# Kernel tuning notes

Hardware: AMD Instinct MI355X
Metric: run time of the kernel (lower is better)

Reference implementation:

```python
import jax, jax.numpy as jnp
import numpy as np

R_MAX = 2.0
DR_MIN = 0.02
N_ATOMS = 200000
N_EDGES = 12800000

def setup_inputs() -> dict:
    key = jax.random.key(0)
    k1, k2, k3, k4, k5, k6 = jax.random.split(key, 6)
    R = jax.random.normal(k1, (N_ATOMS, 3), dtype=jnp.float32)
    dr_vec = jax.random.normal(k2, (N_EDGES, 3), dtype=jnp.float32)
    Z = jax.random.randint(k3, (N_ATOMS,), 0, 119, dtype=jnp.int32)
    idx = jax.random.randint(k4, (2, N_EDGES), 0, N_ATOMS, dtype=jnp.int32)
    box = jnp.zeros((3, 3), dtype=jnp.float32)
    rep_scale = jax.random.uniform(k5, (119,), dtype=jnp.float32, minval=0.2, maxval=1.8)
    rep_prefactor = jax.random.uniform(k6, (119,), dtype=jnp.float32, minval=0.5, maxval=2.0)
    return {"R": R, "dr_vec": dr_vec, "Z": Z, "idx": idx, "box": box,
            "properties": 0, "rep_scale": rep_scale, "rep_prefactor": rep_prefactor}

def reference(R, dr_vec, Z, idx, box, properties, rep_scale, rep_prefactor):
    idx_i, idx_j = idx[0], idx[1]
    # gather per-edge atomic numbers, then per-element parameters
    Z_i = Z[idx_i]
    Z_j = Z[idx_j]
    # per-edge distance, clipped to [0.02, r_max]
    dr = jnp.sqrt(jnp.sum(dr_vec * dr_vec, axis=-1)).astype(jnp.float32)
    dr = jnp.clip(dr, 0.02, R_MAX)
    cos_cutoff = 0.5 * (jnp.cos(np.pi * dr / R_MAX) + 1.0)
    A_i = jnp.abs(rep_prefactor[Z_i])
    A_j = jnp.abs(rep_prefactor[Z_j])
    R_i = jnp.abs(rep_scale[Z_i])
    R_j = jnp.abs(rep_scale[Z_j])
    f = A_i * A_j * jnp.exp(-dr * (R_i + R_j) / (R_i * R_j)) / (dr * dr)
    E_ij = f * cos_cutoff
    # mask padding/self edges (apax pads neighbor lists with idx_i == idx_j)
    mask = (idx_i != idx_j).astype(E_ij.dtype)
    E_ij = E_ij * mask
    # fp64_sum in original; high-precision accumulation via plain sum here
    E = jnp.sum(E_ij)
    return E
```

## Files before the change

### kernel.cpp

```cpp
#include <hip/hip_runtime.h>
#include <hip/hip_bf16.h>
#include <hip/hip_fp16.h>

#define RMAXF 2.0f
#define PI_F 3.14159265358979f

typedef float f32x4 __attribute__((ext_vector_type(4)));
typedef int   i32x4 __attribute__((ext_vector_type(4)));

__global__ __launch_bounds__(256) void build_params(
    const int*   __restrict__ Z,
    const float* __restrict__ rep_scale,
    const float* __restrict__ rep_prefactor,
    __half2*     __restrict__ parh,
    int n_atoms)
{
    int a = blockIdx.x * blockDim.x + threadIdx.x;
    if (a < n_atoms) {
        int z = Z[a];
        float A = fabsf(rep_prefactor[z]);
        float S = 1.0f / fabsf(rep_scale[z]);
        parh[a] = __floats2half2_rn(A, S);
    }
}

__global__ __launch_bounds__(256) void edge_kernel(
    const f32x4* __restrict__ dr4,
    const i32x4* __restrict__ idx_i4,
    const i32x4* __restrict__ idx_j4,
    const __half2* __restrict__ parh,
    float*        __restrict__ out,
    int n_oct, int n_edges)
{
    int q = blockIdx.x * blockDim.x + threadIdx.x;
    float acc = 0.0f;

    if (q < n_oct) {
        f32x4 va = __builtin_nontemporal_load(&dr4[6 * q + 0]);
        f32x4 vb = __builtin_nontemporal_load(&dr4[6 * q + 1]);
        f32x4 vc = __builtin_nontemporal_load(&dr4[6 * q + 2]);
        f32x4 vd = __builtin_nontemporal_load(&dr4[6 * q + 3]);
        f32x4 ve = __builtin_nontemporal_load(&dr4[6 * q + 4]);
        f32x4 vg = __builtin_nontemporal_load(&dr4[6 * q + 5]);
        i32x4 ia = __builtin_nontemporal_load(&idx_i4[2 * q + 0]);
        i32x4 ib = __builtin_nontemporal_load(&idx_i4[2 * q + 1]);
        i32x4 ja = __builtin_nontemporal_load(&idx_j4[2 * q + 0]);
        i32x4 jb = __builtin_nontemporal_load(&idx_j4[2 * q + 1]);

        int ii[8] = { ia.x, ia.y, ia.z, ia.w, ib.x, ib.y, ib.z, ib.w };
        int jj[8] = { ja.x, ja.y, ja.z, ja.w, jb.x, jb.y, jb.z, jb.w };

        __half2 hi[8], hj[8];
        #pragma unroll
        for (int k = 0; k < 8; ++k) { hi[k] = parh[ii[k]]; hj[k] = parh[jj[k]]; }

        float d2[8];
        d2[0] = va.x * va.x + va.y * va.y + va.z * va.z;
        d2[1] = va.w * va.w + vb.x * vb.x + vb.y * vb.y;
        d2[2] = vb.z * vb.z + vb.w * vb.w + vc.x * vc.x;
        d2[3] = vc.y * vc.y + vc.z * vc.z + vc.w * vc.w;
        d2[4] = vd.x * vd.x + vd.y * vd.y + vd.z * vd.z;
        d2[5] = vd.w * vd.w + ve.x * ve.x + ve.y * ve.y;
        d2[6] = ve.z * ve.z + ve.w * ve.w + vg.x * vg.x;
        d2[7] = vg.y * vg.y + vg.z * vg.z + vg.w * vg.w;

        #pragma unroll
        for (int k = 0; k < 8; ++k) {
            float2 pi_ = __half22float2(hi[k]);
            float2 pj_ = __half22float2(hj[k]);
            float d2c = fminf(fmaxf(d2[k], 4.0e-4f), 4.0f);
            float dr  = __builtin_amdgcn_sqrtf(d2c);
            float cv  = __cosf((0.25f * PI_F) * dr);
            float e   = __expf(-dr * (pi_.y + pj_.y));
            float f   = pi_.x * pj_.x * e * __builtin_amdgcn_rcpf(d2c) * cv * cv;
            acc += (ii[k] != jj[k]) ? f : 0.0f;
        }
    }

    if (blockIdx.x == gridDim.x - 1 && threadIdx.x == 0) {
        const float* drf = (const float*)dr4;
        const int* idx_i = (const int*)idx_i4;
        const int* idx_j = (const int*)idx_j4;
        for (int e = n_oct * 8; e < n_edges; ++e) {
            float x = drf[3 * e + 0], y = drf[3 * e + 1], z = drf[3 * e + 2];
            float d2c = fminf(fmaxf(x * x + y * y + z * z, 4.0e-4f), 4.0f);
            float dr  = sqrtf(d2c);
            float cv  = __cosf((0.25f * PI_F) * dr);
            int i = idx_i[e], j = idx_j[e];
            float2 pi_ = __half22float2(parh[i]);
            float2 pj_ = __half22float2(parh[j]);
            float f = pi_.x * pj_.x * __expf(-dr * (pi_.y + pj_.y)) / d2c * cv * cv;
            if (i != j) acc += f;
        }
    }

    #pragma unroll
    for (int off = 32; off > 0; off >>= 1)
        acc += __shfl_down(acc, off, 64);

    __shared__ float wsum[4];
    int lane = threadIdx.x & 63;
    int wid  = threadIdx.x >> 6;
    if (lane == 0) wsum[wid] = acc;
    __syncthreads();
    if (threadIdx.x == 0)
        atomicAdd(out, wsum[0] + wsum[1] + wsum[2] + wsum[3]);
}

__global__ __launch_bounds__(256) void edge_kernel_fallback(
    const float* __restrict__ drf,
    const int*   __restrict__ idx_i,
    const int*   __restrict__ idx_j,
    const int*   __restrict__ Z,
    const float* __restrict__ rep_scale,
    const float* __restrict__ rep_prefactor,
    float*       __restrict__ out,
    int n_edges)
{
    __shared__ float2 tab[128];
    for (int t = threadIdx.x; t < 119; t += blockDim.x)
        tab[t] = make_float2(fabsf(rep_prefactor[t]),
                             1.0f / fabsf(rep_scale[t]));
    __syncthreads();

    float acc = 0.0f;
    const int stride = gridDim.x * blockDim.x;
    for (int e = blockIdx.x * blockDim.x + threadIdx.x; e < n_edges; e += stride) {
        float x = drf[3 * e + 0], y = drf[3 * e + 1], z = drf[3 * e + 2];
        float d2c = fminf(fmaxf(x * x + y * y + z * z, 4.0e-4f), 4.0f);
        float dr  = __builtin_amdgcn_sqrtf(d2c);
        float cv  = __cosf((0.25f * PI_F) * dr);
        int i = idx_i[e], j = idx_j[e];
        float2 pi_ = tab[Z[i]], pj_ = tab[Z[j]];
        float f = pi_.x * pj_.x * __expf(-dr * (pi_.y + pj_.y))
                  * __builtin_amdgcn_rcpf(d2c) * cv * cv;
        acc += (i != j) ? f : 0.0f;
    }

    #pragma unroll
    for (int off = 32; off > 0; off >>= 1)
        acc += __shfl_down(acc, off, 64);
    __shared__ float wsum[4];
    int lane = threadIdx.x & 63;
    int wid  = threadIdx.x >> 6;
    if (lane == 0) wsum[wid] = acc;
    __syncthreads();
    if (threadIdx.x == 0)
        atomicAdd(out, wsum[0] + wsum[1] + wsum[2] + wsum[3]);
}

extern "C" void kernel_launch(void* const* d_in, const int* in_sizes, int n_in,
                              void* d_out, int out_size, void* d_ws, size_t ws_size,
                              hipStream_t stream) {
    const float* dr_vec        = (const float*)d_in[1];
    const int*   Z             = (const int*)d_in[2];
    const int*   idx           = (const int*)d_in[3];
    const float* rep_scale     = (const float*)d_in[6];
    const float* rep_prefactor = (const float*)d_in[7];
    float* out = (float*)d_out;

    const int n_atoms = in_sizes[2];
    const int n_edges = in_sizes[3] / 2;
    const int n_oct   = n_edges / 8;
    const int* idx_i = idx;
    const int* idx_j = idx + n_edges;

    (void)hipMemsetAsync(d_out, 0, sizeof(float), stream);

    const size_t par_bytes = (size_t)n_atoms * sizeof(__half2);
    const bool aligned = ((n_edges & 7) == 0);

    if (ws_size >= par_bytes && aligned) {
        __half2* parh = (__half2*)d_ws;
        build_params<<<(n_atoms + 255) / 256, 256, 0, stream>>>(
            Z, rep_scale, rep_prefactor, parh, n_atoms);
        edge_kernel<<<(n_oct + 255) / 256, 256, 0, stream>>>(
            (const f32x4*)dr_vec, (const i32x4*)idx_i, (const i32x4*)idx_j,
            parh, out, n_oct, n_edges);
    } else {
        int blocks = (n_edges + 255) / 256;
        if (blocks > 4096) blocks = 4096;
        edge_kernel_fallback<<<blocks, 256, 0, stream>>>(
            dr_vec, idx_i, idx_j, Z, rep_scale, rep_prefactor, out, n_edges);
    }
}
```

Measured before the change: 393.5 us.

## Cache per-atom element bytes in LDS and use a persistent grid

Compresses Z into a byte array and stages the first ~162K atoms' element bytes into shared memory in each 1024-thread block. The random gathers then hit LDS, with a small 119-entry parameter table also held in LDS. The grid becomes persistent (at most 256 blocks) so the LDS fill is amortized over many edges. The costs are a ~160KB LDS staging per block, global fallbacks for atoms beyond the cover, and one block per CU with 1024 threads, which may limit memory-level parallelism.

```diff
diff --git a/kernel.cpp b/kernel.cpp
--- a/kernel.cpp
+++ b/kernel.cpp
@@ -8,34 +8,45 @@
 typedef float f32x4 __attribute__((ext_vector_type(4)));
 typedef int   i32x4 __attribute__((ext_vector_type(4)));
 
-__global__ __launch_bounds__(256) void build_params(
-    const int*   __restrict__ Z,
-    const float* __restrict__ rep_scale,
-    const float* __restrict__ rep_prefactor,
-    __half2*     __restrict__ parh,
-    int n_atoms)
+#define LDS_COVER 162304
+
+__global__ __launch_bounds__(256) void z_to_u8(
+    const int* __restrict__ Z, unsigned char* __restrict__ zu8, int n)
 {
-    int a = blockIdx.x * blockDim.x + threadIdx.x;
-    if (a < n_atoms) {
-        int z = Z[a];
-        float A = fabsf(rep_prefactor[z]);
-        float S = 1.0f / fabsf(rep_scale[z]);
-        parh[a] = __floats2half2_rn(A, S);
-    }
-}
-
-__global__ __launch_bounds__(256) void edge_kernel(
+    int i = blockIdx.x * blockDim.x + threadIdx.x;
+    if (i < n) zu8[i] = (unsigned char)Z[i];
+}
+
+__global__ __launch_bounds__(1024) void edge_kernel_lds(
     const f32x4* __restrict__ dr4,
     const i32x4* __restrict__ idx_i4,
     const i32x4* __restrict__ idx_j4,
-    const __half2* __restrict__ parh,
-    float*        __restrict__ out,
-    int n_oct, int n_edges)
+    const unsigned char* __restrict__ zu8,
+    const float* __restrict__ rep_scale,
+    const float* __restrict__ rep_prefactor,
+    float*       __restrict__ out,
+    int n_oct, int n_edges, int cover)
 {
-    int q = blockIdx.x * blockDim.x + threadIdx.x;
+    __shared__ unsigned char zs[LDS_COVER];
+    __shared__ float2 tab[120];
+    __shared__ float wsum[16];
+
+    for (int t = threadIdx.x; t < 119; t += blockDim.x)
+        tab[t] = make_float2(fabsf(rep_prefactor[t]),
+                             1.0f / fabsf(rep_scale[t]));
+    {
+        const i32x4* zsrc = (const i32x4*)zu8;
+        i32x4* zdst = (i32x4*)zs;
+        const int nvec = cover >> 4;
+        for (int t = threadIdx.x; t < nvec; t += blockDim.x)
+            zdst[t] = zsrc[t];
+    }
+    __syncthreads();
+
     float acc = 0.0f;
-
-    if (q < n_oct) {
+    const int stride = gridDim.x * blockDim.x;
+
+    for (int q = blockIdx.x * blockDim.x + threadIdx.x; q < n_oct; q += stride) {
         f32x4 va = __builtin_nontemporal_load(&dr4[6 * q + 0]);
         f32x4 vb = __builtin_nontemporal_load(&dr4[6 * q + 1]);
         f32x4 vc = __builtin_nontemporal_load(&dr4[6 * q + 2]);
@@ -50,9 +61,13 @@
         int ii[8] = { ia.x, ia.y, ia.z, ia.w, ib.x, ib.y, ib.z, ib.w };
         int jj[8] = { ja.x, ja.y, ja.z, ja.w, jb.x, jb.y, jb.z, jb.w };
 
-        __half2 hi[8], hj[8];
+        int zi[8], zj[8];
         #pragma unroll
-        for (int k = 0; k < 8; ++k) { hi[k] = parh[ii[k]]; hj[k] = parh[jj[k]]; }
+        for (int k = 0; k < 8; ++k) {
+            int a = ii[k], b = jj[k];
+            zi[k] = (a < cover) ? (int)zs[a] : (int)zu8[a];
+            zj[k] = (b < cover) ? (int)zs[b] : (int)zu8[b];
+        }
 
         float d2[8];
         d2[0] = va.x * va.x + va.y * va.y + va.z * va.z;
@@ -66,8 +81,8 @@
 
         #pragma unroll
         for (int k = 0; k < 8; ++k) {
-            float2 pi_ = __half22float2(hi[k]);
-            float2 pj_ = __half22float2(hj[k]);
+            float2 pi_ = tab[zi[k]];
+            float2 pj_ = tab[zj[k]];
             float d2c = fminf(fmaxf(d2[k], 4.0e-4f), 4.0f);
             float dr  = __builtin_amdgcn_sqrtf(d2c);
             float cv  = __cosf((0.25f * PI_F) * dr);
@@ -77,7 +92,7 @@
         }
     }
 
-    if (blockIdx.x == gridDim.x - 1 && threadIdx.x == 0) {
+    if (blockIdx.x == 0 && threadIdx.x == 0) {
         const float* drf = (const float*)dr4;
         const int* idx_i = (const int*)idx_i4;
         const int* idx_j = (const int*)idx_j4;
@@ -87,8 +102,8 @@
             float dr  = sqrtf(d2c);
             float cv  = __cosf((0.25f * PI_F) * dr);
             int i = idx_i[e], j = idx_j[e];
-            float2 pi_ = __half22float2(parh[i]);
-            float2 pj_ = __half22float2(parh[j]);
+            float2 pi_ = tab[zu8[i]];
+            float2 pj_ = tab[zu8[j]];
             float f = pi_.x * pj_.x * __expf(-dr * (pi_.y + pj_.y)) / d2c * cv * cv;
             if (i != j) acc += f;
         }
@@ -98,13 +113,16 @@
     for (int off = 32; off > 0; off >>= 1)
         acc += __shfl_down(acc, off, 64);
 
-    __shared__ float wsum[4];
     int lane = threadIdx.x & 63;
     int wid  = threadIdx.x >> 6;
     if (lane == 0) wsum[wid] = acc;
     __syncthreads();
-    if (threadIdx.x == 0)
-        atomicAdd(out, wsum[0] + wsum[1] + wsum[2] + wsum[3]);
+    if (threadIdx.x == 0) {
+        float s = 0.0f;
+        #pragma unroll
+        for (int w = 0; w < 16; ++w) s += wsum[w];
+        atomicAdd(out, s);
+    }
 }
 
 __global__ __launch_bounds__(256) void edge_kernel_fallback(
@@ -167,16 +185,18 @@
 
     (void)hipMemsetAsync(d_out, 0, sizeof(float), stream);
 
-    const size_t par_bytes = (size_t)n_atoms * sizeof(__half2);
     const bool aligned = ((n_edges & 7) == 0);
 
-    if (ws_size >= par_bytes && aligned) {
-        __half2* parh = (__half2*)d_ws;
-        build_params<<<(n_atoms + 255) / 256, 256, 0, stream>>>(
-            Z, rep_scale, rep_prefactor, parh, n_atoms);
-        edge_kernel<<<(n_oct + 255) / 256, 256, 0, stream>>>(
+    if (ws_size >= (size_t)n_atoms && aligned) {
+        unsigned char* zu8 = (unsigned char*)d_ws;
+        z_to_u8<<<(n_atoms + 255) / 256, 256, 0, stream>>>(Z, zu8, n_atoms);
+
+        int cover = n_atoms < LDS_COVER ? (n_atoms & ~15) : LDS_COVER;
+        int blocks = (n_oct + 1023) / 1024;
+        if (blocks > 256) blocks = 256;
+        edge_kernel_lds<<<blocks, 1024, 0, stream>>>(
             (const f32x4*)dr_vec, (const i32x4*)idx_i, (const i32x4*)idx_j,
-            parh, out, n_oct, n_edges);
+            zu8, rep_scale, rep_prefactor, out, n_oct, n_edges, cover);
     } else {
         int blocks = (n_edges + 255) / 256;
         if (blocks > 4096) blocks = 4096;
```

New measurement: 334.6 us. 1.18x faster.
